# Kernel optimization log

Measured on AMD Instinct MI355X. Metric: run time of the kernel, lower is better.

The kernel has to match this reference:

```python
import jax, jax.numpy as jnp
import numpy as np

DIM = 1024
HEADS = 16
DIM_HEAD = 64
CHUNK = 64
INNER = HEADS * DIM_HEAD  # 1024


def setup_inputs() -> dict:
    key = jax.random.key(0)
    k1, k2, k3 = jax.random.split(key, 3)
    x = jax.random.normal(k1, (4, 4096, DIM), dtype=jnp.float32)
    # nn.Linear weights stored as (out, in); apply as x @ W.T
    w_qkv = jax.random.normal(k2, (INNER * 3, DIM), dtype=jnp.float32) * (DIM ** -0.5)
    w_out = jax.random.normal(k3, (DIM, INNER), dtype=jnp.float32) * (INNER ** -0.5)
    b_out = jnp.zeros((DIM,), dtype=jnp.float32)
    return {"x": x, "w_qkv": w_qkv, "w_out": w_out, "b_out": b_out}


def reference(x, w_qkv, w_out, b_out):
    b, n, _ = x.shape
    scale = DIM_HEAD ** -0.5
    qkv = jnp.einsum('bnd,ed->bne', x, w_qkv)  # (b, n, 3*inner)
    q, k, v = jnp.split(qkv, 3, axis=-1)
    nblk = n // CHUNK

    def to_blocks(t):
        # (b, n, h*d) -> (b, h, nblk, c, d)
        t = t.reshape(b, n, HEADS, DIM_HEAD).transpose(0, 2, 1, 3)
        return t.reshape(b, HEADS, nblk, CHUNK, DIM_HEAD)

    qb, kb, vb = to_blocks(q), to_blocks(k), to_blocks(v)
    scores = jnp.einsum('bhgqd,bhgkd->bhgqk', qb, kb) * scale  # block-local
    attn = jax.nn.softmax(scores, axis=-1)
    ob = jnp.einsum('bhgqk,bhgkd->bhgqd', attn, vb)
    out = ob.reshape(b, HEADS, n, DIM_HEAD).transpose(0, 2, 1, 3).reshape(b, n, INNER)
    return jnp.einsum('bne,de->bnd', out, w_out) + b_out
```

## Files before the change

kernel.cpp:

```cpp
#include <hip/hip_runtime.h>
#include <stdint.h>

typedef __attribute__((ext_vector_type(8))) short bf16x8;
typedef __attribute__((ext_vector_type(4))) float f32x4;

__device__ __forceinline__ unsigned short bf16_of(float f) {
  union { float f; uint32_t u; } x; x.f = f;
  uint32_t r = x.u + 0x7fffu + ((x.u >> 16) & 1u);
  return (unsigned short)(r >> 16);
}

#define GLD16(gp, lp) __builtin_amdgcn_global_load_lds( \
    (const __attribute__((address_space(1))) uint32_t*)(gp), \
    (__attribute__((address_space(3))) uint32_t*)(lp), 16, 0, 0)

#define BAR() do { asm volatile("" ::: "memory"); __builtin_amdgcn_s_barrier(); asm volatile("" ::: "memory"); } while (0)

__global__ void cvt_f32_bf16(const float* __restrict__ src,
                             unsigned short* __restrict__ dst, int n4) {
  int i = blockIdx.x * blockDim.x + threadIdx.x;
  int stride = gridDim.x * blockDim.x;
  for (int j = i; j < n4; j += stride) {
    float4 f = ((const float4*)src)[j];
    union { unsigned short s[4]; uint2 v; } u;
    u.s[0] = bf16_of(f.x); u.s[1] = bf16_of(f.y);
    u.s[2] = bf16_of(f.z); u.s[3] = bf16_of(f.w);
    ((uint2*)dst)[j] = u.v;
  }
}

template<int BIAS, int OUTF32, int GW, int NSEG>
__global__ __launch_bounds__(512, 2)
void gemm256h(const unsigned short* __restrict__ A,
              const unsigned short* __restrict__ B,
              void* __restrict__ C, const float* __restrict__ bias,
              int N, int K)
{
  __shared__ __align__(1024) unsigned short sm[65536];
  char* const smb = (char*)sm;
  const int tid = threadIdx.x, w = tid >> 6, lane = tid & 63;
  const int wm = w >> 2, wn = w & 3;
  const int fr = lane & 15, kg = lane >> 4;
  const int swz = (fr & 7) << 4;
  const int srow = lane >> 3, sslot = lane & 7;
  const int cXcd = blockIdx.x & 7, iIdx = blockIdx.x >> 3;
  const int NT_tot = NSEG * 16;

  auto tileMN = [&](int s, int& mt, int& nt) {
    const int T = cXcd * (32 * NSEG) + s * 32 + iIdx;
    const int g = T / (64 * GW), rr = T % (64 * GW);
    mt = rr / GW; nt = g * GW + rr % GW;
  };

  int stOff[2][2];
  #pragma unroll
  for (int h = 0; h < 2; ++h)
    #pragma unroll
    for (int i2 = 0; i2 < 2; ++i2)
      stOff[h][i2] = (h * 128 + (i2 * 8 + w) * 8 + srow) * K + (sslot ^ srow) * 8;

  int curMt, curNt, nxtMt, nxtNt;
  tileMN(0, curMt, curNt);
  nxtMt = curMt; nxtNt = curNt;
  if (NSEG > 1) tileMN(1, nxtMt, nxtNt);
  const unsigned short* aSeg  = A + ((size_t)curMt << 8) * K;
  const unsigned short* bSeg  = B + ((size_t)curNt << 8) * K;
  const unsigned short* aSegN = A + ((size_t)nxtMt << 8) * K;
  const unsigned short* bSegN = B + ((size_t)nxtNt << 8) * K;

  auto STAGEh = [&](const unsigned short* src, int opnd, int half, int parity) {
    char* region = smb + opnd * 65536 + parity * 32768 + half * 16384;
    GLD16(src + stOff[half][0], region + w * 1024);
    GLD16(src + stOff[half][1], region + (8 + w) * 1024);
  };
  auto LDA = [&](char* Ab, int j, int kk) -> bf16x8 {
    const int r = 32 * j + 16 * wm + fr;
    return *(const bf16x8*)(Ab + r * 128 + ((kk * 64 + kg * 16) ^ swz));
  };
  auto LDB = [&](char* Bb, int l, int kk) -> bf16x8 {
    const int r = 64 * l + 16 * wn + fr;
    return *(const bf16x8*)(Bb + r * 128 + ((kk * 64 + kg * 16) ^ swz));
  };

  f32x4 acc[8][4] = {};

  STAGEh(bSeg, 1, 0, 0);
  STAGEh(aSeg, 0, 0, 0);
  STAGEh(bSeg, 1, 1, 0);
  STAGEh(aSeg, 0, 1, 0);

  for (int s = 0; s < NSEG; ++s) {
    for (int tt = 0; tt < 16; ++tt) {
      const int T = s * 16 + tt;
      char* Ab = smb + (T & 1) * 32768;
      char* Bb = smb + 65536 + (T & 1) * 32768;

      asm volatile("s_waitcnt vmcnt(0)" ::: "memory");
      BAR();

      bf16x8 a[4][2], bb[4][2];
      #pragma unroll
      for (int l = 0; l < 4; ++l) { bb[l][0] = LDB(Bb, l, 0); bb[l][1] = LDB(Bb, l, 1); }
      #pragma unroll
      for (int j = 0; j < 4; ++j) { a[j][0] = LDA(Ab, j, 0); a[j][1] = LDA(Ab, j, 1); }

      if (T + 1 < NT_tot) {
        const int p1 = (T + 1) & 1;
        const unsigned short *aS, *bS;
        if (tt < 15) { aS = aSeg + ((tt + 1) << 6); bS = bSeg + ((tt + 1) << 6); }
        else         { aS = aSegN;                  bS = bSegN; }
        STAGEh(bS, 1, 0, p1);
        STAGEh(aS, 0, 0, p1);
        STAGEh(bS, 1, 1, p1);
        STAGEh(aS, 0, 1, p1);
      }

      __builtin_amdgcn_s_setprio(1);
      #pragma unroll
      for (int kk = 0; kk < 2; ++kk)
        #pragma unroll
        for (int j = 0; j < 4; ++j)
          #pragma unroll
          for (int l = 0; l < 4; ++l)
            acc[j][l] = __builtin_amdgcn_mfma_f32_16x16x32_bf16(a[j][kk], bb[l][kk], acc[j][l], 0, 0, 0);
      __builtin_amdgcn_s_setprio(0);

      #pragma unroll
      for (int j = 0; j < 4; ++j) { a[j][0] = LDA(Ab, j + 4, 0); a[j][1] = LDA(Ab, j + 4, 1); }
      __builtin_amdgcn_s_setprio(1);
      #pragma unroll
      for (int kk = 0; kk < 2; ++kk)
        #pragma unroll
        for (int j = 0; j < 4; ++j)
          #pragma unroll
          for (int l = 0; l < 4; ++l)
            acc[j + 4][l] = __builtin_amdgcn_mfma_f32_16x16x32_bf16(a[j][kk], bb[l][kk], acc[j + 4][l], 0, 0, 0);
      __builtin_amdgcn_s_setprio(0);
    }

    const int bm0 = curMt << 8, bn0 = curNt << 8;
    #pragma unroll
    for (int l = 0; l < 4; ++l) {
      const int col = bn0 + 64 * l + 16 * wn + fr;
      float bb2 = 0.0f;
      if (BIAS && OUTF32) bb2 = bias[col];
      #pragma unroll
      for (int j = 0; j < 8; ++j) {
        const int row0 = bm0 + 32 * j + 16 * wm + kg * 4;
        #pragma unroll
        for (int rr = 0; rr < 4; ++rr) {
          if (OUTF32)
            ((float*)C)[(size_t)(row0 + rr) * N + col] = acc[j][l][rr] + bb2;
          else
            ((unsigned short*)C)[(size_t)(row0 + rr) * N + col] = bf16_of(acc[j][l][rr]);
        }
      }
    }
    #pragma unroll
    for (int j = 0; j < 8; ++j)
      #pragma unroll
      for (int l = 0; l < 4; ++l)
        acc[j][l] = f32x4{0.f, 0.f, 0.f, 0.f};

    curMt = nxtMt; curNt = nxtNt;
    aSeg = aSegN; bSeg = bSegN;
    if (s + 2 < NSEG) {
      tileMN(s + 2, nxtMt, nxtNt);
      aSegN = A + ((size_t)nxtMt << 8) * K;
      bSegN = B + ((size_t)nxtNt << 8) * K;
    }
  }
}

__global__ __launch_bounds__(256, 2)
void attn_block(const unsigned short* __restrict__ qkv,
                unsigned short* __restrict__ o)
{
  __shared__ __align__(1024) unsigned short Qs[64 * 64];
  __shared__ __align__(1024) unsigned short Ks[64 * 64];
  __shared__ __align__(1024) unsigned short Vt[64 * 64];
  __shared__ __align__(1024) unsigned short Ps[64 * 64];
  const int tid = threadIdx.x, w = tid >> 6, lane = tid & 63;
  const int g = blockIdx.x, h = blockIdx.y, b = blockIdx.z;
  const size_t mbase = (size_t)b * 4096 + (size_t)g * 64;
  const unsigned short* qg = qkv + mbase * 3072 + h * 64;
  const unsigned short* kgl = qkv + mbase * 3072 + 1024 + h * 64;
  const unsigned short* vg = qkv + mbase * 3072 + 2048 + h * 64;

  #pragma unroll
  for (int i = 0; i < 2; ++i) {
    const int chunk = i * 4 + w;
    const int row = chunk * 8 + (lane >> 3);
    const int c8 = (lane & 7) ^ (row & 7);
    GLD16(qg + (size_t)row * 3072 + c8 * 8, (char*)Qs + chunk * 1024);
    GLD16(kgl + (size_t)row * 3072 + c8 * 8, (char*)Ks + chunk * 1024);
  }
  #pragma unroll
  for (int i = 0; i < 2; ++i) {
    const int c = i * 256 + tid;
    const int n = c >> 3, d0 = (c & 7) * 8;
    bf16x8 v = *(const bf16x8*)(vg + (size_t)n * 3072 + d0);
    #pragma unroll
    for (int j = 0; j < 8; ++j) {
      const int d = d0 + j;
      const int bo = d * 128 + n * 2;
      *(unsigned short*)((char*)Vt + (bo ^ ((d & 7) << 4))) = (unsigned short)v[j];
    }
  }
  __syncthreads();

  const int fr = lane & 15, kg = lane >> 4;
  f32x4 s[4] = {};
  #pragma unroll
  for (int kt = 0; kt < 2; ++kt) {
    const int kb = kt * 64 + kg * 16;
    const int rq = w * 16 + fr;
    bf16x8 aq = *(const bf16x8*)((const char*)Qs + rq * 128 + (kb ^ ((rq & 7) << 4)));
    #pragma unroll
    for (int nf = 0; nf < 4; ++nf) {
      const int rk = nf * 16 + fr;
      bf16x8 bk = *(const bf16x8*)((const char*)Ks + rk * 128 + (kb ^ ((rk & 7) << 4)));
      s[nf] = __builtin_amdgcn_mfma_f32_16x16x32_bf16(aq, bk, s[nf], 0, 0, 0);
    }
  }

  const float scale = 0.125f;
  float inv[4];
  #pragma unroll
  for (int r = 0; r < 4; ++r) {
    float m0 = fmaxf(fmaxf(s[0][r], s[1][r]), fmaxf(s[2][r], s[3][r]));
    #pragma unroll
    for (int d = 1; d < 16; d <<= 1) m0 = fmaxf(m0, __shfl_xor(m0, d));
    float sum = 0.0f;
    #pragma unroll
    for (int nf = 0; nf < 4; ++nf) {
      float p = __expf((s[nf][r] - m0) * scale);
      s[nf][r] = p;
      sum += p;
    }
    #pragma unroll
    for (int d = 1; d < 16; d <<= 1) sum += __shfl_xor(sum, d);
    inv[r] = 1.0f / sum;
  }

  #pragma unroll
  for (int r = 0; r < 4; ++r) {
    const int m = w * 16 + kg * 4 + r;
    #pragma unroll
    for (int nf = 0; nf < 4; ++nf) {
      const int bo = m * 128 + (nf * 16 + fr) * 2;
      *(unsigned short*)((char*)Ps + (bo ^ ((m & 7) << 4))) = bf16_of(s[nf][r] * inv[r]);
    }
  }
  __syncthreads();

  f32x4 oa[4] = {};
  #pragma unroll
  for (int kt = 0; kt < 2; ++kt) {
    const int kb = kt * 64 + kg * 16;
    const int rp = w * 16 + fr;
    bf16x8 ap = *(const bf16x8*)((const char*)Ps + rp * 128 + (kb ^ ((rp & 7) << 4)));
    #pragma unroll
    for (int df = 0; df < 4; ++df) {
      const int rv = df * 16 + fr;
      bf16x8 bv = *(const bf16x8*)((const char*)Vt + rv * 128 + (kb ^ ((rv & 7) << 4)));
      oa[df] = __builtin_amdgcn_mfma_f32_16x16x32_bf16(ap, bv, oa[df], 0, 0, 0);
    }
  }
  #pragma unroll
  for (int df = 0; df < 4; ++df) {
    #pragma unroll
    for (int r = 0; r < 4; ++r) {
      const size_t row = mbase + w * 16 + kg * 4 + r;
      const int col = h * 64 + df * 16 + fr;
      o[row * 1024 + col] = bf16_of(oa[df][r]);
    }
  }
}

extern "C" void kernel_launch(void* const* d_in, const int* in_sizes, int n_in,
                              void* d_out, int out_size, void* d_ws, size_t ws_size,
                              hipStream_t stream) {
  const float* x     = (const float*)d_in[0];
  const float* w_qkv = (const float*)d_in[1];
  const float* w_out = (const float*)d_in[2];
  const float* b_out = (const float*)d_in[3];
  char* ws = (char*)d_ws;
  const size_t SZ_X  = (size_t)16384 * 1024 * 2;
  const size_t SZ_WQ = (size_t)3072 * 1024 * 2;
  const size_t SZ_WO = (size_t)1024 * 1024 * 2;
  unsigned short* xb  = (unsigned short*)ws;
  unsigned short* wqb = (unsigned short*)(ws + SZ_X);
  unsigned short* wob = (unsigned short*)(ws + SZ_X + SZ_WQ);
  unsigned short* qkv = (unsigned short*)(ws + SZ_X + SZ_WQ + SZ_WO);
  unsigned short* ob  = xb;

  cvt_f32_bf16<<<2048, 256, 0, stream>>>(x, xb, 16384 * 1024 / 4);
  cvt_f32_bf16<<<512, 256, 0, stream>>>(w_qkv, wqb, 3072 * 1024 / 4);
  cvt_f32_bf16<<<256, 256, 0, stream>>>(w_out, wob, 1024 * 1024 / 4);
  gemm256h<0,0,6,3><<<dim3(256), 512, 0, stream>>>(xb, wqb, qkv, nullptr, 3072, 1024);
  attn_block<<<dim3(64, 16, 4), 256, 0, stream>>>(qkv, ob);
  gemm256h<1,1,4,1><<<dim3(256), 512, 0, stream>>>(ob, wob, d_out, b_out, 1024, 1024);
}
```

Before: 179.7 us.

## Restructure GEMM main loop into 4-phase ping-pong with depth-2 prefetch

Rewrites the GEMM inner loop so global-to-LDS staging runs two K-tiles ahead instead of one. Each tile's 8x4 MFMA block is split into four quadrant phases separated by barriers, and the staging of the tile two steps ahead is interleaved between them. The goal is to hide global-load latency behind MFMA work and avoid a full vmcnt(0) stall at the top of each iteration. The cost is many more barriers per iteration and tight waitcnt accounting, which risks correctness hazards on the double-buffered LDS regions.

```diff
diff --git a/kernel.cpp b/kernel.cpp
--- a/kernel.cpp
+++ b/kernel.cpp
@@ -15,6 +15,7 @@
     (__attribute__((address_space(3))) uint32_t*)(lp), 16, 0, 0)
 
 #define BAR() do { asm volatile("" ::: "memory"); __builtin_amdgcn_s_barrier(); asm volatile("" ::: "memory"); } while (0)
+#define LGK0() asm volatile("s_waitcnt lgkmcnt(0)" ::: "memory")
 
 __global__ void cvt_f32_bf16(const float* __restrict__ src,
                              unsigned short* __restrict__ dst, int n4) {
@@ -31,7 +32,7 @@
 
 template<int BIAS, int OUTF32, int GW, int NSEG>
 __global__ __launch_bounds__(512, 2)
-void gemm256h(const unsigned short* __restrict__ A,
+void gemm256i(const unsigned short* __restrict__ A,
               const unsigned short* __restrict__ B,
               void* __restrict__ C, const float* __restrict__ bias,
               int N, int K)
@@ -84,58 +85,91 @@
 
   f32x4 acc[8][4] = {};
 
-  STAGEh(bSeg, 1, 0, 0);
-  STAGEh(aSeg, 0, 0, 0);
-  STAGEh(bSeg, 1, 1, 0);
-  STAGEh(aSeg, 0, 1, 0);
+  STAGEh(bSeg, 1, 0, 0); STAGEh(aSeg, 0, 0, 0); STAGEh(bSeg, 1, 1, 0); STAGEh(aSeg, 0, 1, 0);
+  STAGEh(bSeg + 64, 1, 0, 1); STAGEh(aSeg + 64, 0, 0, 1);
+  STAGEh(bSeg + 64, 1, 1, 1); STAGEh(aSeg + 64, 0, 1, 1);
+  asm volatile("s_waitcnt vmcnt(8)" ::: "memory");
+  BAR();
 
   for (int s = 0; s < NSEG; ++s) {
     for (int tt = 0; tt < 16; ++tt) {
       const int T = s * 16 + tt;
       char* Ab = smb + (T & 1) * 32768;
       char* Bb = smb + 65536 + (T & 1) * 32768;
-
-      asm volatile("s_waitcnt vmcnt(0)" ::: "memory");
-      BAR();
-
-      bf16x8 a[4][2], bb[4][2];
-      #pragma unroll
-      for (int l = 0; l < 4; ++l) { bb[l][0] = LDB(Bb, l, 0); bb[l][1] = LDB(Bb, l, 1); }
+      const int p2 = T & 1;
+      const bool doStage = (T + 2 < NT_tot);
+      const unsigned short *aS = aSeg, *bS = bSeg;
+      if (doStage) {
+        if (tt < 14) { aS = aSeg + ((tt + 2) << 6);  bS = bSeg + ((tt + 2) << 6); }
+        else         { aS = aSegN + ((tt - 14) << 6); bS = bSegN + ((tt - 14) << 6); }
+      }
+
+      bf16x8 a[4][2], b0[2][2], b1[2][2];
+
+      #pragma unroll
+      for (int l = 0; l < 2; ++l) { b0[l][0] = LDB(Bb, l, 0); b0[l][1] = LDB(Bb, l, 1); }
       #pragma unroll
       for (int j = 0; j < 4; ++j) { a[j][0] = LDA(Ab, j, 0); a[j][1] = LDA(Ab, j, 1); }
-
-      if (T + 1 < NT_tot) {
-        const int p1 = (T + 1) & 1;
-        const unsigned short *aS, *bS;
-        if (tt < 15) { aS = aSeg + ((tt + 1) << 6); bS = bSeg + ((tt + 1) << 6); }
-        else         { aS = aSegN;                  bS = bSegN; }
-        STAGEh(bS, 1, 0, p1);
-        STAGEh(aS, 0, 0, p1);
-        STAGEh(bS, 1, 1, p1);
-        STAGEh(aS, 0, 1, p1);
-      }
-
+      asm volatile("s_waitcnt lgkmcnt(8)" ::: "memory");
+      BAR();
+      LGK0();
       __builtin_amdgcn_s_setprio(1);
       #pragma unroll
       for (int kk = 0; kk < 2; ++kk)
         #pragma unroll
         for (int j = 0; j < 4; ++j)
           #pragma unroll
-          for (int l = 0; l < 4; ++l)
-            acc[j][l] = __builtin_amdgcn_mfma_f32_16x16x32_bf16(a[j][kk], bb[l][kk], acc[j][l], 0, 0, 0);
+          for (int l = 0; l < 2; ++l)
+            acc[j][l] = __builtin_amdgcn_mfma_f32_16x16x32_bf16(a[j][kk], b0[l][kk], acc[j][l], 0, 0, 0);
       __builtin_amdgcn_s_setprio(0);
-
-      #pragma unroll
-      for (int j = 0; j < 4; ++j) { a[j][0] = LDA(Ab, j + 4, 0); a[j][1] = LDA(Ab, j + 4, 1); }
+      BAR();
+
+      #pragma unroll
+      for (int l = 0; l < 2; ++l) { b1[l][0] = LDB(Bb, l + 2, 0); b1[l][1] = LDB(Bb, l + 2, 1); }
+      if (doStage) STAGEh(aS, 0, 0, p2);
+      BAR();
+      LGK0();
       __builtin_amdgcn_s_setprio(1);
       #pragma unroll
       for (int kk = 0; kk < 2; ++kk)
         #pragma unroll
         for (int j = 0; j < 4; ++j)
           #pragma unroll
-          for (int l = 0; l < 4; ++l)
-            acc[j + 4][l] = __builtin_amdgcn_mfma_f32_16x16x32_bf16(a[j][kk], bb[l][kk], acc[j + 4][l], 0, 0, 0);
+          for (int l = 0; l < 2; ++l)
+            acc[j][l + 2] = __builtin_amdgcn_mfma_f32_16x16x32_bf16(a[j][kk], b1[l][kk], acc[j][l + 2], 0, 0, 0);
       __builtin_amdgcn_s_setprio(0);
+      BAR();
+
+      #pragma unroll
+      for (int j = 0; j < 4; ++j) { a[j][0] = LDA(Ab, j + 4, 0); a[j][1] = LDA(Ab, j + 4, 1); }
+      if (doStage) STAGEh(bS, 1, 0, p2);
+      BAR();
+      LGK0();
+      __builtin_amdgcn_s_setprio(1);
+      #pragma unroll
+      for (int kk = 0; kk < 2; ++kk)
+        #pragma unroll
+        for (int j = 0; j < 4; ++j)
+          #pragma unroll
+          for (int l = 0; l < 2; ++l)
+            acc[j + 4][l + 2] = __builtin_amdgcn_mfma_f32_16x16x32_bf16(a[j][kk], b1[l][kk], acc[j + 4][l + 2], 0, 0, 0);
+      __builtin_amdgcn_s_setprio(0);
+      BAR();
+
+      if (doStage) { STAGEh(bS, 1, 1, p2); STAGEh(aS, 0, 1, p2); }
+      BAR();
+      __builtin_amdgcn_s_setprio(1);
+      #pragma unroll
+      for (int kk = 0; kk < 2; ++kk)
+        #pragma unroll
+        for (int j = 0; j < 4; ++j)
+          #pragma unroll
+          for (int l = 0; l < 2; ++l)
+            acc[j + 4][l] = __builtin_amdgcn_mfma_f32_16x16x32_bf16(a[j][kk], b0[l][kk], acc[j + 4][l], 0, 0, 0);
+      __builtin_amdgcn_s_setprio(0);
+      if (doStage) asm volatile("s_waitcnt vmcnt(8)" ::: "memory");
+      else         asm volatile("s_waitcnt vmcnt(0)" ::: "memory");
+      BAR();
     }
 
     const int bm0 = curMt << 8, bn0 = curNt << 8;
@@ -298,7 +332,7 @@
   cvt_f32_bf16<<<2048, 256, 0, stream>>>(x, xb, 16384 * 1024 / 4);
   cvt_f32_bf16<<<512, 256, 0, stream>>>(w_qkv, wqb, 3072 * 1024 / 4);
   cvt_f32_bf16<<<256, 256, 0, stream>>>(w_out, wob, 1024 * 1024 / 4);
-  gemm256h<0,0,6,3><<<dim3(256), 512, 0, stream>>>(xb, wqb, qkv, nullptr, 3072, 1024);
+  gemm256i<0,0,6,3><<<dim3(256), 512, 0, stream>>>(xb, wqb, qkv, nullptr, 3072, 1024);
   attn_block<<<dim3(64, 16, 4), 256, 0, stream>>>(qkv, ob);
-  gemm256h<1,1,4,1><<<dim3(256), 512, 0, stream>>>(ob, wob, d_out, b_out, 1024, 1024);
-}
+  gemm256i<1,1,4,1><<<dim3(256), 512, 0, stream>>>(ob, wob, d_out, b_out, 1024, 1024);
+}
```

After: 195.5 us. +8.8%, slower.

## Interleave GEMM LDS fragment loads with MFMA quadrants; stage attention output through LDS

Applied to the files above, without the earlier changes.

The GEMM inner loop now issues the next tile's global-to-LDS prefetch before reading fragments. It also splits the B fragments into two halves and reorders the MFMA work into quadrants, so later A-fragment LDS reads overlap with running MFMAs and fewer fragment registers are live at once. The attention kernel now writes its output tile into a swizzled shared buffer and stores it to global memory as contiguous 16-byte vectors, replacing scattered 2-byte stores. This costs an extra 8 KB of shared memory and a barrier per block, and the new MFMA ordering relies on the compiler scheduling the overlap as intended.

```diff
diff --git a/kernel.cpp b/kernel.cpp
--- a/kernel.cpp
+++ b/kernel.cpp
@@ -31,7 +31,7 @@
 
 template<int BIAS, int OUTF32, int GW, int NSEG>
 __global__ __launch_bounds__(512, 2)
-void gemm256h(const unsigned short* __restrict__ A,
+void gemm256j(const unsigned short* __restrict__ A,
               const unsigned short* __restrict__ B,
               void* __restrict__ C, const float* __restrict__ bias,
               int N, int K)
@@ -98,12 +98,6 @@
       asm volatile("s_waitcnt vmcnt(0)" ::: "memory");
       BAR();
 
-      bf16x8 a[4][2], bb[4][2];
-      #pragma unroll
-      for (int l = 0; l < 4; ++l) { bb[l][0] = LDB(Bb, l, 0); bb[l][1] = LDB(Bb, l, 1); }
-      #pragma unroll
-      for (int j = 0; j < 4; ++j) { a[j][0] = LDA(Ab, j, 0); a[j][1] = LDA(Ab, j, 1); }
-
       if (T + 1 < NT_tot) {
         const int p1 = (T + 1) & 1;
         const unsigned short *aS, *bS;
@@ -115,26 +109,67 @@
         STAGEh(aS, 0, 1, p1);
       }
 
+      bf16x8 al[4][2], ah0[4], b0[2][2], b1[2][2];
+
+      #pragma unroll
+      for (int l = 0; l < 2; ++l) b0[l][0] = LDB(Bb, l, 0);
+      #pragma unroll
+      for (int j = 0; j < 4; ++j) al[j][0] = LDA(Ab, j, 0);
+      #pragma unroll
+      for (int l = 0; l < 2; ++l) b0[l][1] = LDB(Bb, l, 1);
+      #pragma unroll
+      for (int j = 0; j < 4; ++j) al[j][1] = LDA(Ab, j, 1);
+      #pragma unroll
+      for (int l = 0; l < 2; ++l) { b1[l][0] = LDB(Bb, l + 2, 0); b1[l][1] = LDB(Bb, l + 2, 1); }
+
       __builtin_amdgcn_s_setprio(1);
       #pragma unroll
       for (int kk = 0; kk < 2; ++kk)
         #pragma unroll
         for (int j = 0; j < 4; ++j)
           #pragma unroll
-          for (int l = 0; l < 4; ++l)
-            acc[j][l] = __builtin_amdgcn_mfma_f32_16x16x32_bf16(a[j][kk], bb[l][kk], acc[j][l], 0, 0, 0);
+          for (int l = 0; l < 2; ++l)
+            acc[j][l] = __builtin_amdgcn_mfma_f32_16x16x32_bf16(al[j][kk], b0[l][kk], acc[j][l], 0, 0, 0);
       __builtin_amdgcn_s_setprio(0);
 
       #pragma unroll
-      for (int j = 0; j < 4; ++j) { a[j][0] = LDA(Ab, j + 4, 0); a[j][1] = LDA(Ab, j + 4, 1); }
+      for (int j = 0; j < 4; ++j) ah0[j] = LDA(Ab, j + 4, 0);
+
       __builtin_amdgcn_s_setprio(1);
       #pragma unroll
       for (int kk = 0; kk < 2; ++kk)
         #pragma unroll
         for (int j = 0; j < 4; ++j)
           #pragma unroll
-          for (int l = 0; l < 4; ++l)
-            acc[j + 4][l] = __builtin_amdgcn_mfma_f32_16x16x32_bf16(a[j][kk], bb[l][kk], acc[j + 4][l], 0, 0, 0);
+          for (int l = 0; l < 2; ++l)
+            acc[j][l + 2] = __builtin_amdgcn_mfma_f32_16x16x32_bf16(al[j][kk], b1[l][kk], acc[j][l + 2], 0, 0, 0);
+      __builtin_amdgcn_s_setprio(0);
+
+      #pragma unroll
+      for (int j = 0; j < 4; ++j) al[j][0] = LDA(Ab, j + 4, 1);
+
+      __builtin_amdgcn_s_setprio(1);
+      #pragma unroll
+      for (int j = 0; j < 4; ++j)
+        #pragma unroll
+        for (int l = 0; l < 2; ++l)
+          acc[j + 4][l + 2] = __builtin_amdgcn_mfma_f32_16x16x32_bf16(ah0[j], b1[l][0], acc[j + 4][l + 2], 0, 0, 0);
+      #pragma unroll
+      for (int j = 0; j < 4; ++j)
+        #pragma unroll
+        for (int l = 0; l < 2; ++l)
+          acc[j + 4][l + 2] = __builtin_amdgcn_mfma_f32_16x16x32_bf16(al[j][0], b1[l][1], acc[j + 4][l + 2], 0, 0, 0);
+
+      #pragma unroll
+      for (int j = 0; j < 4; ++j)
+        #pragma unroll
+        for (int l = 0; l < 2; ++l)
+          acc[j + 4][l] = __builtin_amdgcn_mfma_f32_16x16x32_bf16(ah0[j], b0[l][0], acc[j + 4][l], 0, 0, 0);
+      #pragma unroll
+      for (int j = 0; j < 4; ++j)
+        #pragma unroll
+        for (int l = 0; l < 2; ++l)
+          acc[j + 4][l] = __builtin_amdgcn_mfma_f32_16x16x32_bf16(al[j][0], b0[l][1], acc[j + 4][l], 0, 0, 0);
       __builtin_amdgcn_s_setprio(0);
     }
 
@@ -180,6 +215,7 @@
   __shared__ __align__(1024) unsigned short Ks[64 * 64];
   __shared__ __align__(1024) unsigned short Vt[64 * 64];
   __shared__ __align__(1024) unsigned short Ps[64 * 64];
+  __shared__ __align__(1024) unsigned short Os[64 * 64];
   const int tid = threadIdx.x, w = tid >> 6, lane = tid & 63;
   const int g = blockIdx.x, h = blockIdx.y, b = blockIdx.z;
   const size_t mbase = (size_t)b * 4096 + (size_t)g * 64;
@@ -267,14 +303,27 @@
       oa[df] = __builtin_amdgcn_mfma_f32_16x16x32_bf16(ap, bv, oa[df], 0, 0, 0);
     }
   }
+
   #pragma unroll
   for (int df = 0; df < 4; ++df) {
     #pragma unroll
     for (int r = 0; r < 4; ++r) {
-      const size_t row = mbase + w * 16 + kg * 4 + r;
-      const int col = h * 64 + df * 16 + fr;
-      o[row * 1024 + col] = bf16_of(oa[df][r]);
-    }
+      const int m = w * 16 + kg * 4 + r;
+      const int bo = m * 128 + (df * 16 + fr) * 2;
+      *(unsigned short*)((char*)Os + (bo ^ ((m & 7) << 4))) = bf16_of(oa[df][r]);
+    }
+  }
+  __syncthreads();
+  {
+    const int row = tid >> 2;
+    const int sb = (tid & 3) * 32;
+    const int sw = (row & 7) << 4;
+    char* rp = (char*)Os + row * 128;
+    uint4 v0 = *(uint4*)(rp + (sb ^ sw));
+    uint4 v1 = *(uint4*)(rp + ((sb + 16) ^ sw));
+    char* op = (char*)(o + (mbase + row) * 1024 + h * 64) + sb;
+    *(uint4*)op = v0;
+    *(uint4*)(op + 16) = v1;
   }
 }
 
@@ -298,7 +347,7 @@
   cvt_f32_bf16<<<2048, 256, 0, stream>>>(x, xb, 16384 * 1024 / 4);
   cvt_f32_bf16<<<512, 256, 0, stream>>>(w_qkv, wqb, 3072 * 1024 / 4);
   cvt_f32_bf16<<<256, 256, 0, stream>>>(w_out, wob, 1024 * 1024 / 4);
-  gemm256h<0,0,6,3><<<dim3(256), 512, 0, stream>>>(xb, wqb, qkv, nullptr, 3072, 1024);
+  gemm256j<0,0,6,3><<<dim3(256), 512, 0, stream>>>(xb, wqb, qkv, nullptr, 3072, 1024);
   attn_block<<<dim3(64, 16, 4), 256, 0, stream>>>(qkv, ob);
-  gemm256h<1,1,4,1><<<dim3(256), 512, 0, stream>>>(ob, wob, d_out, b_out, 1024, 1024);
-}
+  gemm256j<1,1,4,1><<<dim3(256), 512, 0, stream>>>(ob, wob, d_out, b_out, 1024, 1024);
+}
```

Result: slower. 184.0 us (+2.4%).

## Fuse fp32-to-bf16 conversion of x into QKV GEMM and coalesce attention output stores

Applied to the files above, without the earlier changes.

The QKV GEMM now reads fp32 activations straight from global memory into registers, converts them to bf16, and writes them into LDS. This removes the separate conversion kernel for x and its 32 MB bf16 round trip. The attention kernel now stages its output tile in swizzled LDS and writes rows with 16-byte stores instead of scattered 2-byte stores. In exchange, each GEMM iteration loads twice the A bytes through registers, and a register-to-LDS write plus a wait sits on the critical path between compute steps.

```diff
diff --git a/kernel.cpp b/kernel.cpp
--- a/kernel.cpp
+++ b/kernel.cpp
@@ -29,13 +29,14 @@
   }
 }
 
-template<int BIAS, int OUTF32, int GW, int NSEG>
+template<int AF32, int BIAS, int OUTF32, int GW, int NSEG>
 __global__ __launch_bounds__(512, 2)
-void gemm256h(const unsigned short* __restrict__ A,
-              const unsigned short* __restrict__ B,
+void gemm256k(const void* __restrict__ Av, const unsigned short* __restrict__ Bv,
               void* __restrict__ C, const float* __restrict__ bias,
               int N, int K)
 {
+  const unsigned short* A16 = (const unsigned short*)Av;
+  const float* A32 = (const float*)Av;
   __shared__ __align__(1024) unsigned short sm[65536];
   char* const smb = (char*)sm;
   const int tid = threadIdx.x, w = tid >> 6, lane = tid & 63;
@@ -63,16 +64,48 @@
   tileMN(0, curMt, curNt);
   nxtMt = curMt; nxtNt = curNt;
   if (NSEG > 1) tileMN(1, nxtMt, nxtNt);
-  const unsigned short* aSeg  = A + ((size_t)curMt << 8) * K;
-  const unsigned short* bSeg  = B + ((size_t)curNt << 8) * K;
-  const unsigned short* aSegN = A + ((size_t)nxtMt << 8) * K;
-  const unsigned short* bSegN = B + ((size_t)nxtNt << 8) * K;
-
-  auto STAGEh = [&](const unsigned short* src, int opnd, int half, int parity) {
-    char* region = smb + opnd * 65536 + parity * 32768 + half * 16384;
+  size_t aSegO  = ((size_t)curMt << 8) * (size_t)K;
+  size_t aSegNO = ((size_t)nxtMt << 8) * (size_t)K;
+  const unsigned short* bSeg  = Bv + ((size_t)curNt << 8) * K;
+  const unsigned short* bSegN = Bv + ((size_t)nxtNt << 8) * K;
+
+  auto STAGEB = [&](const unsigned short* src, int half, int parity) {
+    char* region = smb + 65536 + parity * 32768 + half * 16384;
     GLD16(src + stOff[half][0], region + w * 1024);
     GLD16(src + stOff[half][1], region + (8 + w) * 1024);
   };
+  auto STAGEA16 = [&](const unsigned short* src, int half, int parity) {
+    char* region = smb + parity * 32768 + half * 16384;
+    GLD16(src + stOff[half][0], region + w * 1024);
+    GLD16(src + stOff[half][1], region + (8 + w) * 1024);
+  };
+
+  float4 af[2][2][2];
+  auto LOADA32 = [&](const float* src) {
+    #pragma unroll
+    for (int h2 = 0; h2 < 2; ++h2)
+      #pragma unroll
+      for (int i2 = 0; i2 < 2; ++i2) {
+        const float* p = src + stOff[h2][i2];
+        af[h2][i2][0] = *(const float4*)p;
+        af[h2][i2][1] = *(const float4*)(p + 4);
+      }
+  };
+  auto WRITEA32 = [&](int parity) {
+    #pragma unroll
+    for (int h2 = 0; h2 < 2; ++h2)
+      #pragma unroll
+      for (int i2 = 0; i2 < 2; ++i2) {
+        union { unsigned short s[8]; uint4 v; } u;
+        u.s[0] = bf16_of(af[h2][i2][0].x); u.s[1] = bf16_of(af[h2][i2][0].y);
+        u.s[2] = bf16_of(af[h2][i2][0].z); u.s[3] = bf16_of(af[h2][i2][0].w);
+        u.s[4] = bf16_of(af[h2][i2][1].x); u.s[5] = bf16_of(af[h2][i2][1].y);
+        u.s[6] = bf16_of(af[h2][i2][1].z); u.s[7] = bf16_of(af[h2][i2][1].w);
+        char* region = smb + parity * 32768 + h2 * 16384;
+        *(uint4*)(region + (i2 * 8 + w) * 1024 + lane * 16) = u.v;
+      }
+  };
+
   auto LDA = [&](char* Ab, int j, int kk) -> bf16x8 {
     const int r = 32 * j + 16 * wm + fr;
     return *(const bf16x8*)(Ab + r * 128 + ((kk * 64 + kg * 16) ^ swz));
@@ -84,10 +117,16 @@
 
   f32x4 acc[8][4] = {};
 
-  STAGEh(bSeg, 1, 0, 0);
-  STAGEh(aSeg, 0, 0, 0);
-  STAGEh(bSeg, 1, 1, 0);
-  STAGEh(aSeg, 0, 1, 0);
+  STAGEB(bSeg, 0, 0); STAGEB(bSeg, 1, 0);
+  if (AF32) {
+    LOADA32(A32 + aSegO);
+    asm volatile("s_waitcnt vmcnt(0)" ::: "memory");
+    WRITEA32(0);
+    asm volatile("s_waitcnt lgkmcnt(0)" ::: "memory");
+  } else {
+    STAGEA16(A16 + aSegO, 0, 0); STAGEA16(A16 + aSegO, 1, 0);
+    asm volatile("s_waitcnt vmcnt(0)" ::: "memory");
+  }
 
   for (int s = 0; s < NSEG; ++s) {
     for (int tt = 0; tt < 16; ++tt) {
@@ -95,7 +134,6 @@
       char* Ab = smb + (T & 1) * 32768;
       char* Bb = smb + 65536 + (T & 1) * 32768;
 
-      asm volatile("s_waitcnt vmcnt(0)" ::: "memory");
       BAR();
 
       bf16x8 a[4][2], bb[4][2];
@@ -104,15 +142,18 @@
       #pragma unroll
       for (int j = 0; j < 4; ++j) { a[j][0] = LDA(Ab, j, 0); a[j][1] = LDA(Ab, j, 1); }
 
-      if (T + 1 < NT_tot) {
+      const bool hasNext = (T + 1 < NT_tot);
+      if (hasNext) {
         const int p1 = (T + 1) & 1;
-        const unsigned short *aS, *bS;
-        if (tt < 15) { aS = aSeg + ((tt + 1) << 6); bS = bSeg + ((tt + 1) << 6); }
-        else         { aS = aSegN;                  bS = bSegN; }
-        STAGEh(bS, 1, 0, p1);
-        STAGEh(aS, 0, 0, p1);
-        STAGEh(bS, 1, 1, p1);
-        STAGEh(aS, 0, 1, p1);
+        const unsigned short* bS = (tt < 15) ? bSeg + ((tt + 1) << 6) : bSegN;
+        STAGEB(bS, 0, p1); STAGEB(bS, 1, p1);
+        if (AF32) {
+          const size_t aO = (tt < 15) ? aSegO + ((size_t)(tt + 1) << 6) : aSegNO;
+          LOADA32(A32 + aO);
+        } else {
+          const unsigned short* aS = A16 + ((tt < 15) ? aSegO + ((size_t)(tt + 1) << 6) : aSegNO);
+          STAGEA16(aS, 0, p1); STAGEA16(aS, 1, p1);
+        }
       }
 
       __builtin_amdgcn_s_setprio(1);
@@ -136,6 +177,12 @@
           for (int l = 0; l < 4; ++l)
             acc[j + 4][l] = __builtin_amdgcn_mfma_f32_16x16x32_bf16(a[j][kk], bb[l][kk], acc[j + 4][l], 0, 0, 0);
       __builtin_amdgcn_s_setprio(0);
+
+      asm volatile("s_waitcnt vmcnt(0)" ::: "memory");
+      if (AF32 && hasNext) {
+        WRITEA32((T + 1) & 1);
+        asm volatile("s_waitcnt lgkmcnt(0)" ::: "memory");
+      }
     }
 
     const int bm0 = curMt << 8, bn0 = curNt << 8;
@@ -163,11 +210,11 @@
         acc[j][l] = f32x4{0.f, 0.f, 0.f, 0.f};
 
     curMt = nxtMt; curNt = nxtNt;
-    aSeg = aSegN; bSeg = bSegN;
+    aSegO = aSegNO; bSeg = bSegN;
     if (s + 2 < NSEG) {
       tileMN(s + 2, nxtMt, nxtNt);
-      aSegN = A + ((size_t)nxtMt << 8) * K;
-      bSegN = B + ((size_t)nxtNt << 8) * K;
+      aSegNO = ((size_t)nxtMt << 8) * (size_t)K;
+      bSegN = Bv + ((size_t)nxtNt << 8) * K;
     }
   }
 }
@@ -180,6 +227,7 @@
   __shared__ __align__(1024) unsigned short Ks[64 * 64];
   __shared__ __align__(1024) unsigned short Vt[64 * 64];
   __shared__ __align__(1024) unsigned short Ps[64 * 64];
+  __shared__ __align__(1024) unsigned short Os[64 * 64];
   const int tid = threadIdx.x, w = tid >> 6, lane = tid & 63;
   const int g = blockIdx.x, h = blockIdx.y, b = blockIdx.z;
   const size_t mbase = (size_t)b * 4096 + (size_t)g * 64;
@@ -267,14 +315,27 @@
       oa[df] = __builtin_amdgcn_mfma_f32_16x16x32_bf16(ap, bv, oa[df], 0, 0, 0);
     }
   }
+
   #pragma unroll
   for (int df = 0; df < 4; ++df) {
     #pragma unroll
     for (int r = 0; r < 4; ++r) {
-      const size_t row = mbase + w * 16 + kg * 4 + r;
-      const int col = h * 64 + df * 16 + fr;
-      o[row * 1024 + col] = bf16_of(oa[df][r]);
-    }
+      const int m = w * 16 + kg * 4 + r;
+      const int bo = m * 128 + (df * 16 + fr) * 2;
+      *(unsigned short*)((char*)Os + (bo ^ ((m & 7) << 4))) = bf16_of(oa[df][r]);
+    }
+  }
+  __syncthreads();
+  {
+    const int row = tid >> 2;
+    const int sb = (tid & 3) * 32;
+    const int sw = (row & 7) << 4;
+    char* rp = (char*)Os + row * 128;
+    uint4 v0 = *(uint4*)(rp + (sb ^ sw));
+    uint4 v1 = *(uint4*)(rp + ((sb + 16) ^ sw));
+    char* op = (char*)(o + (mbase + row) * 1024 + h * 64) + sb;
+    *(uint4*)op = v0;
+    *(uint4*)(op + 16) = v1;
   }
 }
 
@@ -286,19 +347,17 @@
   const float* w_out = (const float*)d_in[2];
   const float* b_out = (const float*)d_in[3];
   char* ws = (char*)d_ws;
-  const size_t SZ_X  = (size_t)16384 * 1024 * 2;
-  const size_t SZ_WQ = (size_t)3072 * 1024 * 2;
-  const size_t SZ_WO = (size_t)1024 * 1024 * 2;
-  unsigned short* xb  = (unsigned short*)ws;
-  unsigned short* wqb = (unsigned short*)(ws + SZ_X);
-  unsigned short* wob = (unsigned short*)(ws + SZ_X + SZ_WQ);
-  unsigned short* qkv = (unsigned short*)(ws + SZ_X + SZ_WQ + SZ_WO);
-  unsigned short* ob  = xb;
-
-  cvt_f32_bf16<<<2048, 256, 0, stream>>>(x, xb, 16384 * 1024 / 4);
+  const size_t SZ_WQ  = (size_t)3072 * 1024 * 2;
+  const size_t SZ_WO  = (size_t)1024 * 1024 * 2;
+  const size_t SZ_QKV = (size_t)16384 * 3072 * 2;
+  unsigned short* wqb = (unsigned short*)ws;
+  unsigned short* wob = (unsigned short*)(ws + SZ_WQ);
+  unsigned short* qkv = (unsigned short*)(ws + SZ_WQ + SZ_WO);
+  unsigned short* ob  = (unsigned short*)(ws + SZ_WQ + SZ_WO + SZ_QKV);
+
   cvt_f32_bf16<<<512, 256, 0, stream>>>(w_qkv, wqb, 3072 * 1024 / 4);
   cvt_f32_bf16<<<256, 256, 0, stream>>>(w_out, wob, 1024 * 1024 / 4);
-  gemm256h<0,0,6,3><<<dim3(256), 512, 0, stream>>>(xb, wqb, qkv, nullptr, 3072, 1024);
+  gemm256k<1,0,0,6,3><<<dim3(256), 512, 0, stream>>>(x, wqb, qkv, nullptr, 3072, 1024);
   attn_block<<<dim3(64, 16, 4), 256, 0, stream>>>(qkv, ob);
-  gemm256h<1,1,4,1><<<dim3(256), 512, 0, stream>>>(ob, wob, d_out, b_out, 1024, 1024);
-}
+  gemm256k<0,1,1,4,1><<<dim3(256), 512, 0, stream>>>(ob, wob, d_out, b_out, 1024, 1024);
+}
```

Result: slower. 201.2 us (+11.9%).
